# Kernel optimization log

Measured on AMD Instinct MI355X. Metric: run time of the kernel, lower is better.

The kernel has to match this reference:

```python
import jax, jax.numpy as jnp
import numpy as np

SPATIAL_SHAPES = ((100, 100), (50, 50), (25, 25), (13, 13))
B, C, NH, NL, NP, DFF = 4, 256, 8, 4, 4, 1024
HD = C // NH
L = sum(h * w for h, w in SPATIAL_SHAPES)  # 13294


def _xavier(key, shape):
    s = (6.0 / (shape[0] + shape[1])) ** 0.5
    return jax.random.uniform(key, shape, jnp.float32, -s, s)


def setup_inputs():
    key = jax.random.key(0)
    ks = jax.random.split(key, 12)
    ss = jnp.array(SPATIAL_SHAPES, jnp.int32)
    lsi = jnp.concatenate([jnp.zeros((1,), jnp.int32), jnp.cumsum(ss[:, 0] * ss[:, 1])[:-1].astype(jnp.int32)])
    return {
        "query": jax.random.normal(ks[0], (B, L, C), jnp.float32),
        "query_pos": jax.random.normal(ks[1], (B, L, C), jnp.float32),
        "reference_points": jax.random.uniform(ks[2], (B, L, NL, 2), jnp.float32),
        "spatial_shapes": ss,
        "level_start_index": lsi,
        "v_W": _xavier(ks[3], (C, C)), "v_b": jnp.zeros((C,), jnp.float32),
        "off_W": 0.01 * jax.random.normal(ks[4], (C, NH * NL * NP * 2), jnp.float32),
        "off_b": 0.1 * jax.random.normal(ks[5], (NH * NL * NP * 2,), jnp.float32),
        "aw_W": 0.01 * jax.random.normal(ks[6], (C, NH * NL * NP), jnp.float32),
        "aw_b": jnp.zeros((NH * NL * NP,), jnp.float32),
        "out_W": _xavier(ks[7], (C, C)), "out_b": jnp.zeros((C,), jnp.float32),
        "ln1_g": jnp.ones((C,), jnp.float32), "ln1_b": jnp.zeros((C,), jnp.float32),
        "lin1_W": _xavier(ks[8], (C, DFF)), "lin1_b": jnp.zeros((DFF,), jnp.float32),
        "lin2_W": _xavier(ks[9], (DFF, C)), "lin2_b": jnp.zeros((C,), jnp.float32),
        "ln2_g": jnp.ones((C,), jnp.float32), "ln2_b": jnp.zeros((C,), jnp.float32),
    }


def _layer_norm(x, g, b):
    mu = x.mean(-1, keepdims=True)
    var = ((x - mu) ** 2).mean(-1, keepdims=True)
    return (x - mu) * jax.lax.rsqrt(var + 1e-5) * g + b


def _msda(q, value, reference_points, v_W, v_b, off_W, off_b, aw_W, aw_b, out_W, out_b):
    # value projection, split heads -> [B, NH, L, HD]
    v = (value @ v_W + v_b).reshape(B, L, NH, HD).transpose(0, 2, 1, 3)
    off = (q @ off_W + off_b).reshape(B, L, NH, NL, NP, 2)
    aw = jax.nn.softmax((q @ aw_W + aw_b).reshape(B, L, NH, NL * NP), axis=-1)
    aw = aw.reshape(B, L, NH, NL, NP).transpose(0, 2, 1, 3, 4)  # [B,NH,L,NL,NP]
    # offset normalizer is (W, H) per level, matching (x, y) coords
    norm = jnp.array([[w, h] for h, w in SPATIAL_SHAPES], q.dtype)
    loc = reference_points[:, :, None, :, None, :] + off / norm[None, None, None, :, None, :]
    loc = loc.transpose(0, 2, 1, 3, 4, 5)  # [B,NH,L,NL,NP,2]
    acc = jnp.zeros((B, NH, L, HD), q.dtype)
    start = 0
    for l, (H_, W_) in enumerate(SPATIAL_SHAPES):
        v_l = jax.lax.dynamic_slice_in_dim(v, start, H_ * W_, axis=2)  # [B,NH,HW,HD]
        # grid_sample(align_corners=False): pixel = loc*size - 0.5
        x = loc[:, :, :, l, :, 0] * W_ - 0.5  # [B,NH,L,NP]
        y = loc[:, :, :, l, :, 1] * H_ - 0.5
        x0 = jnp.floor(x); y0 = jnp.floor(y)
        lx = x - x0; ly = y - y0
        x0i = x0.astype(jnp.int32); y0i = y0.astype(jnp.int32)

        def corner(yi, xi, w):
            valid = (yi >= 0) & (yi < H_) & (xi >= 0) & (xi < W_)  # zero padding
            idx = jnp.clip(yi, 0, H_ - 1) * W_ + jnp.clip(xi, 0, W_ - 1)
            g = jnp.take_along_axis(v_l, idx.reshape(B, NH, L * NP, 1), axis=2)
            g = g.reshape(B, NH, L, NP, HD)
            return g * (w * valid)[..., None]

        s = (corner(y0i, x0i, (1 - ly) * (1 - lx))
             + corner(y0i, x0i + 1, (1 - ly) * lx)
             + corner(y0i + 1, x0i, ly * (1 - lx))
             + corner(y0i + 1, x0i + 1, ly * lx))  # [B,NH,L,NP,HD]
        acc = acc + (s * aw[:, :, :, l, :, None]).sum(3)
        start += H_ * W_
    out = acc.transpose(0, 2, 1, 3).reshape(B, L, C)
    return out @ out_W + out_b


def _forward(query, query_pos, reference_points, v_W, v_b, off_W, off_b, aw_W, aw_b,
             out_W, out_b, ln1_g, ln1_b, lin1_W, lin1_b, lin2_W, lin2_b, ln2_g, ln2_b):
    q = query + query_pos
    src2 = _msda(q, query, reference_points, v_W, v_b, off_W, off_b, aw_W, aw_b, out_W, out_b)
    x = _layer_norm(query + src2, ln1_g, ln1_b)
    ffn = jax.nn.relu(x @ lin1_W + lin1_b) @ lin2_W + lin2_b
    return _layer_norm(x + ffn, ln2_g, ln2_b)


def reference(query, query_pos, reference_points, spatial_shapes, level_start_index,
              v_W, v_b, off_W, off_b, aw_W, aw_b, out_W, out_b,
              ln1_g, ln1_b, lin1_W, lin1_b, lin2_W, lin2_b, ln2_g, ln2_b):
    # spatial_shapes / level_start_index are consistent with the static SPATIAL_SHAPES
    # constant (shapes must be static for reshapes under jit).
    return _forward(query, query_pos, reference_points, v_W, v_b, off_W, off_b, aw_W, aw_b,
                    out_W, out_b, ln1_g, ln1_b, lin1_W, lin1_b, lin2_W, lin2_b, ln2_g, ln2_b)
```

## Files before the change

kernel.cpp:

```cpp
#include <hip/hip_runtime.h>
#include <hip/hip_bf16.h>
#include <cstddef>

constexpr int Ll   = 13294;
constexpr int NROW = 4 * Ll;
constexpr int MP   = 53248;

typedef __bf16       bf8v __attribute__((ext_vector_type(8)));
typedef __bf16       bf2v __attribute__((ext_vector_type(2)));
typedef float        f4v  __attribute__((ext_vector_type(4)));
typedef unsigned int u4v  __attribute__((ext_vector_type(4)));

#if defined(__has_builtin)
#  if __has_builtin(__builtin_amdgcn_fdot2_f32_bf16)
#    define HAVE_DOT2_BF16 1
#  endif
#endif
#ifndef HAVE_DOT2_BF16
#  define HAVE_DOT2_BF16 0
#endif

__device__ __forceinline__ void xcd_remap(int& m0, int& n0)
{
    const int nwg  = gridDim.x * gridDim.y;
    const int flat = blockIdx.y * gridDim.x + blockIdx.x;
    const int w    = (flat & 7) * (nwg >> 3) + (flat >> 3);
    n0 = (w % gridDim.x) * 128;
    m0 = (w / gridDim.x) * 128;
}

template<bool RELU, bool OUTF, bool OUTB>
__global__ __launch_bounds__(256)
void gemm_mfma(const __hip_bfloat16* __restrict__ A, const __hip_bfloat16* __restrict__ Bt,
               const float* __restrict__ bias, const float* __restrict__ bias2,
               float* __restrict__ Cf, __hip_bfloat16* __restrict__ Cb,
               int M, int N, int K)
{
    __shared__ __hip_bfloat16 As[2][128 * 32];
    __shared__ __hip_bfloat16 Bs[2][128 * 32];
    const int tid  = threadIdx.x;
    const int wid  = tid >> 6;
    const int lane = tid & 63;
    int m0, n0;
    xcd_remap(m0, n0);
    const int wm = wid >> 1, wn = wid & 1;
    const int fr = lane & 15, fq = lane >> 4;
    const int sr = lane >> 2;
    const int sc = (lane & 3) * 8;

    f4v acc[4][4] = {};

    for (int k0 = 0; k0 < K; k0 += 64) {
        #pragma unroll
        for (int h = 0; h < 2; ++h) {
            #pragma unroll
            for (int i = 0; i < 2; ++i) {
                const int s = wid * 2 + i;
                const __hip_bfloat16* sa = A  + (size_t)(m0 + s * 16 + sr) * K + k0 + h * 32 + sc;
                const __hip_bfloat16* sb = Bt + (size_t)(n0 + s * 16 + sr) * K + k0 + h * 32 + sc;
                __builtin_amdgcn_global_load_lds(
                    (const __attribute__((address_space(1))) void*)sa,
                    (__attribute__((address_space(3))) void*)&As[h][s * 512], 16, 0, 0);
                __builtin_amdgcn_global_load_lds(
                    (const __attribute__((address_space(1))) void*)sb,
                    (__attribute__((address_space(3))) void*)&Bs[h][s * 512], 16, 0, 0);
            }
        }
        __syncthreads();

        #pragma unroll
        for (int h = 0; h < 2; ++h) {
            bf8v a[4], b[4];
            #pragma unroll
            for (int r = 0; r < 4; ++r) {
                a[r] = __builtin_bit_cast(bf8v, *(const u4v*)&As[h][(wm * 64 + r * 16 + fr) * 32 + fq * 8]);
                b[r] = __builtin_bit_cast(bf8v, *(const u4v*)&Bs[h][(wn * 64 + r * 16 + fr) * 32 + fq * 8]);
            }
            #pragma unroll
            for (int nr = 0; nr < 4; ++nr)
                #pragma unroll
                for (int mr = 0; mr < 4; ++mr)
                    acc[nr][mr] = __builtin_amdgcn_mfma_f32_16x16x32_bf16(b[nr], a[mr], acc[nr][mr], 0, 0, 0);
        }
        __syncthreads();
    }

    #pragma unroll
    for (int nr = 0; nr < 4; ++nr) {
        const int colbase = n0 + wn * 64 + nr * 16 + fq * 4;
        const float* bp = (bias2 != nullptr && colbase >= 256) ? (bias2 - 256) : bias;
        const float4 b4 = *(const float4*)&bp[colbase];
        #pragma unroll
        for (int mr = 0; mr < 4; ++mr) {
            const int row = m0 + wm * 64 + mr * 16 + fr;
            f4v v = acc[nr][mr];
            v[0] += b4.x; v[1] += b4.y; v[2] += b4.z; v[3] += b4.w;
            if (RELU) {
                v[0] = fmaxf(v[0], 0.f); v[1] = fmaxf(v[1], 0.f);
                v[2] = fmaxf(v[2], 0.f); v[3] = fmaxf(v[3], 0.f);
            }
            if (OUTF)
                *(float4*)&Cf[(size_t)row * N + colbase] = make_float4(v[0], v[1], v[2], v[3]);
            if (OUTB) {
                union { ushort4 u; __hip_bfloat16 h[4]; } pk;
                pk.h[0] = __float2bfloat16(v[0]); pk.h[1] = __float2bfloat16(v[1]);
                pk.h[2] = __float2bfloat16(v[2]); pk.h[3] = __float2bfloat16(v[3]);
                *(ushort4*)&Cb[(size_t)row * N + colbase] = pk.u;
            }
        }
    }
}

template<bool STOREB, bool RESB>
__global__ __launch_bounds__(256)
void gemm_ln(const __hip_bfloat16* __restrict__ A, const __hip_bfloat16* __restrict__ Bt,
             const float* __restrict__ bias,
             const float* __restrict__ resF, const __hip_bfloat16* __restrict__ resB,
             int Mres,
             const float* __restrict__ g, const float* __restrict__ be,
             float* __restrict__ outF, int MstoreF,
             __hip_bfloat16* __restrict__ outB,
             int K)
{
    __shared__ __hip_bfloat16 As[2][64 * 32];
    __shared__ __hip_bfloat16 Bs[2][256 * 32];
    __shared__ float red[2][64][2];
    const int tid  = threadIdx.x;
    const int wid  = tid >> 6;
    const int lane = tid & 63;
    const int m0 = blockIdx.x * 64;
    const int wm = wid >> 1, wn = wid & 1;
    const int fr = lane & 15, fq = lane >> 4;
    const int sr = lane >> 2;
    const int sc = (lane & 3) * 8;

    f4v acc[8][2] = {};

    for (int k0 = 0; k0 < K; k0 += 64) {
        #pragma unroll
        for (int h = 0; h < 2; ++h) {
            {
                const __hip_bfloat16* sa = A + (size_t)(m0 + wid * 16 + sr) * K + k0 + h * 32 + sc;
                __builtin_amdgcn_global_load_lds(
                    (const __attribute__((address_space(1))) void*)sa,
                    (__attribute__((address_space(3))) void*)&As[h][wid * 512], 16, 0, 0);
            }
            #pragma unroll
            for (int i = 0; i < 4; ++i) {
                const int s = wid * 4 + i;
                const __hip_bfloat16* sb = Bt + (size_t)(s * 16 + sr) * K + k0 + h * 32 + sc;
                __builtin_amdgcn_global_load_lds(
                    (const __attribute__((address_space(1))) void*)sb,
                    (__attribute__((address_space(3))) void*)&Bs[h][s * 512], 16, 0, 0);
            }
        }
        __syncthreads();

        #pragma unroll
        for (int h = 0; h < 2; ++h) {
            bf8v a[2], b[8];
            #pragma unroll
            for (int r = 0; r < 2; ++r)
                a[r] = __builtin_bit_cast(bf8v, *(const u4v*)&As[h][(wm * 32 + r * 16 + fr) * 32 + fq * 8]);
            #pragma unroll
            for (int r = 0; r < 8; ++r)
                b[r] = __builtin_bit_cast(bf8v, *(const u4v*)&Bs[h][(wn * 128 + r * 16 + fr) * 32 + fq * 8]);
            #pragma unroll
            for (int nr = 0; nr < 8; ++nr)
                #pragma unroll
                for (int mr = 0; mr < 2; ++mr)
                    acc[nr][mr] = __builtin_amdgcn_mfma_f32_16x16x32_bf16(b[nr], a[mr], acc[nr][mr], 0, 0, 0);
        }
        __syncthreads();
    }

    float s2[2] = {}, q2[2] = {};
    #pragma unroll
    for (int nr = 0; nr < 8; ++nr) {
        const int colbase = wn * 128 + nr * 16 + fq * 4;
        const float4 b4 = *(const float4*)&bias[colbase];
        #pragma unroll
        for (int mr = 0; mr < 2; ++mr) {
            const int row = m0 + wm * 32 + mr * 16 + fr;
            f4v x = acc[nr][mr];
            x[0] += b4.x; x[1] += b4.y; x[2] += b4.z; x[3] += b4.w;
            if (RESB) {
                const ushort4 r4 = *(const ushort4*)&resB[(size_t)row * 256 + colbase];
                x[0] += __builtin_bit_cast(float, (unsigned)r4.x << 16);
                x[1] += __builtin_bit_cast(float, (unsigned)r4.y << 16);
                x[2] += __builtin_bit_cast(float, (unsigned)r4.z << 16);
                x[3] += __builtin_bit_cast(float, (unsigned)r4.w << 16);
            } else if (row < Mres) {
                const float4 r4 = *(const float4*)&resF[(size_t)row * 256 + colbase];
                x[0] += r4.x; x[1] += r4.y; x[2] += r4.z; x[3] += r4.w;
            }
            acc[nr][mr] = x;
            s2[mr] += x[0] + x[1] + x[2] + x[3];
            q2[mr] += x[0]*x[0] + x[1]*x[1] + x[2]*x[2] + x[3]*x[3];
        }
    }
    #pragma unroll
    for (int mr = 0; mr < 2; ++mr) {
        s2[mr] += __shfl_xor(s2[mr], 16, 64);
        q2[mr] += __shfl_xor(q2[mr], 16, 64);
        s2[mr] += __shfl_xor(s2[mr], 32, 64);
        q2[mr] += __shfl_xor(q2[mr], 32, 64);
    }
    if (fq == 0) {
        #pragma unroll
        for (int mr = 0; mr < 2; ++mr) {
            red[wn][wm * 32 + mr * 16 + fr][0] = s2[mr];
            red[wn][wm * 32 + mr * 16 + fr][1] = q2[mr];
        }
    }
    __syncthreads();
    float mean[2], rinv[2];
    #pragma unroll
    for (int mr = 0; mr < 2; ++mr) {
        const int r = wm * 32 + mr * 16 + fr;
        const float ss = red[0][r][0] + red[1][r][0];
        const float qq = red[0][r][1] + red[1][r][1];
        mean[mr] = ss * (1.f / 256.f);
        const float var = qq * (1.f / 256.f) - mean[mr] * mean[mr];
        rinv[mr] = rsqrtf(var + 1e-5f);
    }
    #pragma unroll
    for (int nr = 0; nr < 8; ++nr) {
        const int colbase = wn * 128 + nr * 16 + fq * 4;
        const float4 g4 = *(const float4*)&g[colbase];
        const float4 e4 = *(const float4*)&be[colbase];
        #pragma unroll
        for (int mr = 0; mr < 2; ++mr) {
            const int row = m0 + wm * 32 + mr * 16 + fr;
            const f4v x = acc[nr][mr];
            float y0 = (x[0] - mean[mr]) * rinv[mr] * g4.x + e4.x;
            float y1 = (x[1] - mean[mr]) * rinv[mr] * g4.y + e4.y;
            float y2 = (x[2] - mean[mr]) * rinv[mr] * g4.z + e4.z;
            float y3 = (x[3] - mean[mr]) * rinv[mr] * g4.w + e4.w;
            if (row < MstoreF)
                *(float4*)&outF[(size_t)row * 256 + colbase] = make_float4(y0, y1, y2, y3);
            if (STOREB) {
                union { ushort4 u; __hip_bfloat16 h[4]; } pk;
                pk.h[0] = __float2bfloat16(y0); pk.h[1] = __float2bfloat16(y1);
                pk.h[2] = __float2bfloat16(y2); pk.h[3] = __float2bfloat16(y3);
                *(ushort4*)&outB[(size_t)row * 256 + colbase] = pk.u;
            }
        }
    }
}

__global__ __launch_bounds__(256)
void prep_weights(const float* __restrict__ vW, const float* __restrict__ offW,
                  const float* __restrict__ awW, const float* __restrict__ outW,
                  const float* __restrict__ w1, const float* __restrict__ w2,
                  __hip_bfloat16* __restrict__ vWt, __hip_bfloat16* __restrict__ catWt,
                  __hip_bfloat16* __restrict__ outWt, __hip_bfloat16* __restrict__ w1t,
                  __hip_bfloat16* __restrict__ w2t)
{
    int i = blockIdx.x * 256 + threadIdx.x;
    if (i < 65536) { const int n = i >> 8, k = i & 255;
        vWt[i] = __float2bfloat16(vW[(size_t)k * 256 + n]); return; }
    i -= 65536;
    if (i < 98304) { const int n = i >> 8, k = i & 255;
        catWt[i] = __float2bfloat16(n < 256 ? offW[(size_t)k * 256 + n]
                                            : awW[(size_t)k * 128 + n - 256]); return; }
    i -= 98304;
    if (i < 65536) { const int n = i >> 8, k = i & 255;
        outWt[i] = __float2bfloat16(outW[(size_t)k * 256 + n]); return; }
    i -= 65536;
    if (i < 262144) { const int n = i >> 8, k = i & 255;
        w1t[i] = __float2bfloat16(w1[(size_t)k * 1024 + n]); return; }
    i -= 262144;
    { const int n = i >> 10, k = i & 1023;
        w2t[i] = __float2bfloat16(w2[(size_t)k * 256 + n]); }
}

__global__ __launch_bounds__(256)
void cvt_both(const float* __restrict__ q, const float* __restrict__ qp,
              __hip_bfloat16* __restrict__ qb, __hip_bfloat16* __restrict__ qpb)
{
    const int i   = blockIdx.x * 256 + threadIdx.x;
    const int row = i >> 5;
    union { u4v u; __hip_bfloat16 h[8]; } p1, p2;
    if (row >= NROW) {
        u4v z = {0u, 0u, 0u, 0u};
        p1.u = z; p2.u = z;
    } else {
        const size_t e = (size_t)i * 8;
        float4 x0 = *(const float4*)&q[e];
        float4 x1 = *(const float4*)&q[e + 4];
        float4 y0 = *(const float4*)&qp[e];
        float4 y1 = *(const float4*)&qp[e + 4];
        p1.h[0] = __float2bfloat16(x0.x); p1.h[1] = __float2bfloat16(x0.y);
        p1.h[2] = __float2bfloat16(x0.z); p1.h[3] = __float2bfloat16(x0.w);
        p1.h[4] = __float2bfloat16(x1.x); p1.h[5] = __float2bfloat16(x1.y);
        p1.h[6] = __float2bfloat16(x1.z); p1.h[7] = __float2bfloat16(x1.w);
        p2.h[0] = __float2bfloat16(x0.x + y0.x); p2.h[1] = __float2bfloat16(x0.y + y0.y);
        p2.h[2] = __float2bfloat16(x0.z + y0.z); p2.h[3] = __float2bfloat16(x0.w + y0.w);
        p2.h[4] = __float2bfloat16(x1.x + y1.x); p2.h[5] = __float2bfloat16(x1.y + y1.y);
        p2.h[6] = __float2bfloat16(x1.z + y1.z); p2.h[7] = __float2bfloat16(x1.w + y1.w);
    }
    *(u4v*)&qb[(size_t)i * 8]  = p1.u;
    *(u4v*)&qpb[(size_t)i * 8] = p2.u;
}

__device__ __forceinline__ float blo(unsigned u) { return __builtin_bit_cast(float, u << 16); }
__device__ __forceinline__ float bhi(unsigned u) { return __builtin_bit_cast(float, u & 0xffff0000u); }

__global__ __launch_bounds__(256)
void msda_sample5(const __hip_bfloat16* __restrict__ v, const __hip_bfloat16* __restrict__ cat,
                  const float* __restrict__ refp, __hip_bfloat16* __restrict__ accO)
{
    __shared__ int      sIdx[1024][4];
    __shared__ unsigned sWpk[1024][2];
    int blk;
    {
        const int nwg  = gridDim.x;
        const int q    = nwg >> 3;
        const int r    = nwg & 7;
        const int xcd  = blockIdx.x & 7;
        const int off  = blockIdx.x >> 3;
        blk = (xcd < r ? xcd * (q + 1) : r * (q + 1) + (xcd - r) * q) + off;
    }
    const int row0 = blk * 8;
    const int tid  = threadIdx.x;

    #pragma unroll
    for (int it = 0; it < 4; ++it) {
        const int item = it * 256 + tid;
        const int p = item & 15, h = (item >> 4) & 7, r = item >> 7;
        const int row = row0 + r;
        const int lvl = p >> 2;
        const float logit = __bfloat162float(cat[(size_t)row * 384 + 256 + h * 16 + p]);
        float mx = logit;
        #pragma unroll
        for (int o = 1; o < 16; o <<= 1) mx = fmaxf(mx, __shfl_xor(mx, o, 64));
        const float e = __expf(logit - mx);
        float s = e;
        #pragma unroll
        for (int o = 1; o < 16; o <<= 1) s += __shfl_xor(s, o, 64);
        const float aw = e / s;

        const int Hs_[4] = {100, 50, 25, 13};
        const int Ss[4]  = {0, 10000, 12500, 13125};
        const int   Wl = Hs_[lvl];
        const float Wf = (float)Wl;
        const float ox = __bfloat162float(cat[(size_t)row * 384 + h * 32 + p * 2 + 0]);
        const float oy = __bfloat162float(cat[(size_t)row * 384 + h * 32 + p * 2 + 1]);
        const float rx = refp[(size_t)row * 8 + lvl * 2 + 0];
        const float ry = refp[(size_t)row * 8 + lvl * 2 + 1];
        const float x = (rx + ox / Wf) * Wf - 0.5f;
        const float y = (ry + oy / Wf) * Wf - 0.5f;
        const float x0f = floorf(x), y0f = floorf(y);
        const float lx = x - x0f, ly = y - y0f;
        const int x0 = (int)x0f, y0 = (int)y0f;
        const int b = row / Ll;
        const int vbase = b * Ll + Ss[lvl];
        int ixr[4]; unsigned short wb[4];
        #pragma unroll
        for (int c = 0; c < 4; ++c) {
            const int cy = c >> 1, cx = c & 1;
            const int yi = y0 + cy, xi = x0 + cx;
            const bool ok = (yi >= 0) & (yi < Wl) & (xi >= 0) & (xi < Wl);
            const int yc = min(max(yi, 0), Wl - 1);
            const int xc = min(max(xi, 0), Wl - 1);
            const float wt = (cy ? ly : 1.f - ly) * (cx ? lx : 1.f - lx);
            ixr[c] = (vbase + yc * Wl + xc) * 512;
            const __hip_bfloat16 hw = __float2bfloat16(ok ? aw * wt : 0.f);
            wb[c] = __builtin_bit_cast(unsigned short, hw);
        }
        const int item2 = (item & ~15) | ((item & 15) ^ h);
        *(int4*)&sIdx[item2][0] = make_int4(ixr[0], ixr[1], ixr[2], ixr[3]);
        sWpk[item2][0] = (unsigned)wb[0] | ((unsigned)wb[1] << 16);
        sWpk[item2][1] = (unsigned)wb[2] | ((unsigned)wb[3] << 16);
    }
    __syncthreads();

    const int r   = tid >> 5;
    const int h   = (tid >> 2) & 7;
    const int oct = tid & 3;
    const int row = row0 + r;
    const char* vB = (const char*)v + (h * 32 + oct * 8) * 2;
    const int ibase = r * 128 + h * 16;
    float acc[8] = {};
    #pragma unroll
    for (int i = 0; i < 16; ++i) {
        const int idx = ibase + (i ^ h);
        const int4  ix = *(const int4*)&sIdx[idx][0];
        const uint2 wp = *(const uint2*)&sWpk[idx][0];
        u4v u0 = *(const u4v*)(vB + (unsigned)ix.x);
        u4v u1 = *(const u4v*)(vB + (unsigned)ix.y);
        u4v u2 = *(const u4v*)(vB + (unsigned)ix.z);
        u4v u3 = *(const u4v*)(vB + (unsigned)ix.w);
#if HAVE_DOT2_BF16
        const bf2v w01 = __builtin_bit_cast(bf2v, wp.x);
        const bf2v w23 = __builtin_bit_cast(bf2v, wp.y);
        #pragma unroll
        for (int q = 0; q < 4; ++q) {
            const unsigned lo01 = __builtin_amdgcn_perm(u1[q], u0[q], 0x05040100u);
            const unsigned hi01 = __builtin_amdgcn_perm(u1[q], u0[q], 0x07060302u);
            const unsigned lo23 = __builtin_amdgcn_perm(u3[q], u2[q], 0x05040100u);
            const unsigned hi23 = __builtin_amdgcn_perm(u3[q], u2[q], 0x07060302u);
            acc[2*q]   = __builtin_amdgcn_fdot2_f32_bf16(__builtin_bit_cast(bf2v, lo01), w01, acc[2*q],   false);
            acc[2*q]   = __builtin_amdgcn_fdot2_f32_bf16(__builtin_bit_cast(bf2v, lo23), w23, acc[2*q],   false);
            acc[2*q+1] = __builtin_amdgcn_fdot2_f32_bf16(__builtin_bit_cast(bf2v, hi01), w01, acc[2*q+1], false);
            acc[2*q+1] = __builtin_amdgcn_fdot2_f32_bf16(__builtin_bit_cast(bf2v, hi23), w23, acc[2*q+1], false);
        }
#else
        const float w0 = blo(wp.x), w1 = bhi(wp.x);
        const float w2 = blo(wp.y), w3 = bhi(wp.y);
        #pragma unroll
        for (int q = 0; q < 4; ++q) {
            acc[2*q]   = fmaf(w0, blo(u0[q]), acc[2*q]);
            acc[2*q+1] = fmaf(w0, bhi(u0[q]), acc[2*q+1]);
            acc[2*q]   = fmaf(w1, blo(u1[q]), acc[2*q]);
            acc[2*q+1] = fmaf(w1, bhi(u1[q]), acc[2*q+1]);
            acc[2*q]   = fmaf(w2, blo(u2[q]), acc[2*q]);
            acc[2*q+1] = fmaf(w2, bhi(u2[q]), acc[2*q+1]);
            acc[2*q]   = fmaf(w3, blo(u3[q]), acc[2*q]);
            acc[2*q+1] = fmaf(w3, bhi(u3[q]), acc[2*q+1]);
        }
#endif
    }
    union { u4v u; __hip_bfloat16 hh[8]; } pk;
    #pragma unroll
    for (int q = 0; q < 8; ++q) pk.hh[q] = __float2bfloat16(acc[q]);
    *(u4v*)&accO[(size_t)row * 256 + h * 32 + oct * 8] = pk.u;
}

extern "C" void kernel_launch(void* const* d_in, const int* in_sizes, int n_in,
                              void* d_out, int out_size, void* d_ws, size_t ws_size,
                              hipStream_t stream)
{
    (void)in_sizes; (void)n_in; (void)out_size; (void)ws_size;
    const float* query = (const float*)d_in[0];
    const float* qpos  = (const float*)d_in[1];
    const float* refp  = (const float*)d_in[2];
    const float* v_W   = (const float*)d_in[5];
    const float* v_b   = (const float*)d_in[6];
    const float* off_W = (const float*)d_in[7];
    const float* off_b = (const float*)d_in[8];
    const float* aw_W  = (const float*)d_in[9];
    const float* aw_b  = (const float*)d_in[10];
    const float* out_W = (const float*)d_in[11];
    const float* out_b = (const float*)d_in[12];
    const float* ln1g  = (const float*)d_in[13];
    const float* ln1b  = (const float*)d_in[14];
    const float* w1    = (const float*)d_in[15];
    const float* b1    = (const float*)d_in[16];
    const float* w2    = (const float*)d_in[17];
    const float* b2    = (const float*)d_in[18];
    const float* ln2g  = (const float*)d_in[19];
    const float* ln2b  = (const float*)d_in[20];
    float* out = (float*)d_out;

    char* ws = (char*)d_ws;
    constexpr size_t HALF_B = (size_t)MP * 256 * 2;
    constexpr size_t HBUF_B = (size_t)MP * 1024 * 2;
    __hip_bfloat16* hbuf = (__hip_bfloat16*)ws;
    __hip_bfloat16* qb   = (__hip_bfloat16*)ws;
    __hip_bfloat16* qpb  = (__hip_bfloat16*)(ws + HALF_B);
    __hip_bfloat16* catb = (__hip_bfloat16*)(ws + 2 * HALF_B);
    __hip_bfloat16* vbuf = (__hip_bfloat16*)(ws + HBUF_B);
    __hip_bfloat16* accb = qpb;
    __hip_bfloat16* xb   = vbuf;
    char* wsw = ws + HBUF_B + HALF_B;
    __hip_bfloat16* vWt   = (__hip_bfloat16*)(wsw);
    __hip_bfloat16* catWt = (__hip_bfloat16*)(wsw + 131072);
    __hip_bfloat16* outWt = (__hip_bfloat16*)(wsw + 327680);
    __hip_bfloat16* w1t   = (__hip_bfloat16*)(wsw + 458752);
    __hip_bfloat16* w2t   = (__hip_bfloat16*)(wsw + 983040);

    dim3 blk(256);

    prep_weights<<<2944, blk, 0, stream>>>(v_W, off_W, aw_W, out_W, w1, w2,
                                           vWt, catWt, outWt, w1t, w2t);
    cvt_both<<<MP / 8, blk, 0, stream>>>(query, qpos, qb, qpb);

    gemm_mfma<false, false, true><<<dim3(2, MP / 128), blk, 0, stream>>>(
        qb, vWt, v_b, nullptr, nullptr, vbuf, MP, 256, 256);
    gemm_mfma<false, false, true><<<dim3(3, MP / 128), blk, 0, stream>>>(
        qpb, catWt, off_b, aw_b, nullptr, catb, MP, 384, 256);

    msda_sample5<<<NROW / 8, blk, 0, stream>>>(vbuf, catb, refp, accb);

    gemm_ln<true, true><<<MP / 64, blk, 0, stream>>>(
        accb, outWt, out_b, nullptr, qb, MP, ln1g, ln1b,
        nullptr, 0, xb, 256);

    gemm_mfma<true, false, true><<<dim3(8, MP / 128), blk, 0, stream>>>(
        xb, w1t, b1, nullptr, nullptr, hbuf, MP, 1024, 256);

    gemm_ln<false, true><<<MP / 64, blk, 0, stream>>>(
        hbuf, w2t, b2, nullptr, xb, MP, ln2g, ln2b,
        out, NROW, nullptr, 1024);
}
```

Measured before the change: 343.4 us.

## Merge prep kernels, fuse projection GEMMs, software-pipeline MSDA sampling loads

Three changes ship together. The weight-prep and query-conversion kernels are merged into one launch, and the value and offset/attention projection GEMMs share a single grid with an XCD-aware tile remap, cutting launches and tail idle time. The MSDA sampling loop is now double-buffered: gathers for the next two sampling points are issued before the current ones are consumed, and sched_barriers stop the compiler from reordering them. This raises register pressure and adds branch divergence between the two GEMM shapes in the fused grid.

```diff
diff --git a/kernel.cpp b/kernel.cpp
--- a/kernel.cpp
+++ b/kernel.cpp
@@ -30,19 +30,16 @@
 }
 
 template<bool RELU, bool OUTF, bool OUTB>
-__global__ __launch_bounds__(256)
-void gemm_mfma(const __hip_bfloat16* __restrict__ A, const __hip_bfloat16* __restrict__ Bt,
+__device__ __forceinline__
+void gemm_body(const __hip_bfloat16* __restrict__ A, const __hip_bfloat16* __restrict__ Bt,
                const float* __restrict__ bias, const float* __restrict__ bias2,
                float* __restrict__ Cf, __hip_bfloat16* __restrict__ Cb,
-               int M, int N, int K)
-{
-    __shared__ __hip_bfloat16 As[2][128 * 32];
-    __shared__ __hip_bfloat16 Bs[2][128 * 32];
+               int N, int K, int m0, int n0,
+               __hip_bfloat16 (*As)[128 * 32], __hip_bfloat16 (*Bs)[128 * 32])
+{
     const int tid  = threadIdx.x;
     const int wid  = tid >> 6;
     const int lane = tid & 63;
-    int m0, n0;
-    xcd_remap(m0, n0);
     const int wm = wid >> 1, wn = wid & 1;
     const int fr = lane & 15, fq = lane >> 4;
     const int sr = lane >> 2;
@@ -109,6 +106,41 @@
             }
         }
     }
+}
+
+template<bool RELU, bool OUTF, bool OUTB>
+__global__ __launch_bounds__(256)
+void gemm_mfma(const __hip_bfloat16* __restrict__ A, const __hip_bfloat16* __restrict__ Bt,
+               const float* __restrict__ bias, const float* __restrict__ bias2,
+               float* __restrict__ Cf, __hip_bfloat16* __restrict__ Cb,
+               int M, int N, int K)
+{
+    __shared__ __hip_bfloat16 As[2][128 * 32];
+    __shared__ __hip_bfloat16 Bs[2][128 * 32];
+    int m0, n0;
+    xcd_remap(m0, n0);
+    gemm_body<RELU, OUTF, OUTB>(A, Bt, bias, bias2, Cf, Cb, N, K, m0, n0, As, Bs);
+}
+
+__global__ __launch_bounds__(256)
+void gemm_proj_pair(const __hip_bfloat16* __restrict__ qb, const __hip_bfloat16* __restrict__ qpb,
+                    const __hip_bfloat16* __restrict__ vWt, const __hip_bfloat16* __restrict__ catWt,
+                    const float* __restrict__ v_b, const float* __restrict__ off_b,
+                    const float* __restrict__ aw_b,
+                    __hip_bfloat16* __restrict__ vbuf, __hip_bfloat16* __restrict__ catb)
+{
+    __shared__ __hip_bfloat16 As[2][128 * 32];
+    __shared__ __hip_bfloat16 Bs[2][128 * 32];
+    const int nwg  = 2080;
+    const int flat = blockIdx.x;
+    const int w    = (flat & 7) * (nwg >> 3) + (flat >> 3);
+    const int n    = w % 5, m = w / 5;
+    if (n < 2)
+        gemm_body<false, false, true>(qb, vWt, v_b, nullptr,
+                                      nullptr, vbuf, 256, 256, m * 128, n * 128, As, Bs);
+    else
+        gemm_body<false, false, true>(qpb, catWt, off_b, aw_b,
+                                      nullptr, catb, 384, 256, m * 128, (n - 2) * 128, As, Bs);
 }
 
 template<bool STOREB, bool RESB>
@@ -250,36 +282,35 @@
 }
 
 __global__ __launch_bounds__(256)
-void prep_weights(const float* __restrict__ vW, const float* __restrict__ offW,
-                  const float* __restrict__ awW, const float* __restrict__ outW,
-                  const float* __restrict__ w1, const float* __restrict__ w2,
-                  __hip_bfloat16* __restrict__ vWt, __hip_bfloat16* __restrict__ catWt,
-                  __hip_bfloat16* __restrict__ outWt, __hip_bfloat16* __restrict__ w1t,
-                  __hip_bfloat16* __restrict__ w2t)
-{
-    int i = blockIdx.x * 256 + threadIdx.x;
-    if (i < 65536) { const int n = i >> 8, k = i & 255;
-        vWt[i] = __float2bfloat16(vW[(size_t)k * 256 + n]); return; }
-    i -= 65536;
-    if (i < 98304) { const int n = i >> 8, k = i & 255;
-        catWt[i] = __float2bfloat16(n < 256 ? offW[(size_t)k * 256 + n]
-                                            : awW[(size_t)k * 128 + n - 256]); return; }
-    i -= 98304;
-    if (i < 65536) { const int n = i >> 8, k = i & 255;
-        outWt[i] = __float2bfloat16(outW[(size_t)k * 256 + n]); return; }
-    i -= 65536;
-    if (i < 262144) { const int n = i >> 8, k = i & 255;
-        w1t[i] = __float2bfloat16(w1[(size_t)k * 1024 + n]); return; }
-    i -= 262144;
-    { const int n = i >> 10, k = i & 1023;
-        w2t[i] = __float2bfloat16(w2[(size_t)k * 256 + n]); }
-}
-
-__global__ __launch_bounds__(256)
-void cvt_both(const float* __restrict__ q, const float* __restrict__ qp,
+void prep_all(const float* __restrict__ vW, const float* __restrict__ offW,
+              const float* __restrict__ awW, const float* __restrict__ outW,
+              const float* __restrict__ w1, const float* __restrict__ w2,
+              __hip_bfloat16* __restrict__ vWt, __hip_bfloat16* __restrict__ catWt,
+              __hip_bfloat16* __restrict__ outWt, __hip_bfloat16* __restrict__ w1t,
+              __hip_bfloat16* __restrict__ w2t,
+              const float* __restrict__ q, const float* __restrict__ qp,
               __hip_bfloat16* __restrict__ qb, __hip_bfloat16* __restrict__ qpb)
 {
-    const int i   = blockIdx.x * 256 + threadIdx.x;
+    if (blockIdx.x < 2944) {
+        int i = blockIdx.x * 256 + threadIdx.x;
+        if (i < 65536) { const int n = i >> 8, k = i & 255;
+            vWt[i] = __float2bfloat16(vW[(size_t)k * 256 + n]); return; }
+        i -= 65536;
+        if (i < 98304) { const int n = i >> 8, k = i & 255;
+            catWt[i] = __float2bfloat16(n < 256 ? offW[(size_t)k * 256 + n]
+                                                : awW[(size_t)k * 128 + n - 256]); return; }
+        i -= 98304;
+        if (i < 65536) { const int n = i >> 8, k = i & 255;
+            outWt[i] = __float2bfloat16(outW[(size_t)k * 256 + n]); return; }
+        i -= 65536;
+        if (i < 262144) { const int n = i >> 8, k = i & 255;
+            w1t[i] = __float2bfloat16(w1[(size_t)k * 1024 + n]); return; }
+        i -= 262144;
+        { const int n = i >> 10, k = i & 1023;
+            w2t[i] = __float2bfloat16(w2[(size_t)k * 256 + n]); }
+        return;
+    }
+    const int i   = (blockIdx.x - 2944) * 256 + threadIdx.x;
     const int row = i >> 5;
     union { u4v u; __hip_bfloat16 h[8]; } p1, p2;
     if (row >= NROW) {
@@ -307,8 +338,50 @@
 __device__ __forceinline__ float blo(unsigned u) { return __builtin_bit_cast(float, u << 16); }
 __device__ __forceinline__ float bhi(unsigned u) { return __builtin_bit_cast(float, u & 0xffff0000u); }
 
+#if HAVE_DOT2_BF16
+#define MSDA_CONSUME(WP, U0, U1, U2, U3) do { \
+    const bf2v w01_ = __builtin_bit_cast(bf2v, (WP).x); \
+    const bf2v w23_ = __builtin_bit_cast(bf2v, (WP).y); \
+    _Pragma("unroll") \
+    for (int q_ = 0; q_ < 4; ++q_) { \
+        const unsigned lo01_ = __builtin_amdgcn_perm((U1)[q_], (U0)[q_], 0x05040100u); \
+        const unsigned hi01_ = __builtin_amdgcn_perm((U1)[q_], (U0)[q_], 0x07060302u); \
+        const unsigned lo23_ = __builtin_amdgcn_perm((U3)[q_], (U2)[q_], 0x05040100u); \
+        const unsigned hi23_ = __builtin_amdgcn_perm((U3)[q_], (U2)[q_], 0x07060302u); \
+        acc[2*q_]   = __builtin_amdgcn_fdot2_f32_bf16(__builtin_bit_cast(bf2v, lo01_), w01_, acc[2*q_],   false); \
+        acc[2*q_]   = __builtin_amdgcn_fdot2_f32_bf16(__builtin_bit_cast(bf2v, lo23_), w23_, acc[2*q_],   false); \
+        acc[2*q_+1] = __builtin_amdgcn_fdot2_f32_bf16(__builtin_bit_cast(bf2v, hi01_), w01_, acc[2*q_+1], false); \
+        acc[2*q_+1] = __builtin_amdgcn_fdot2_f32_bf16(__builtin_bit_cast(bf2v, hi23_), w23_, acc[2*q_+1], false); \
+    } } while (0)
+#else
+#define MSDA_CONSUME(WP, U0, U1, U2, U3) do { \
+    const float w0_ = blo((WP).x), w1_ = bhi((WP).x); \
+    const float w2_ = blo((WP).y), w3_ = bhi((WP).y); \
+    _Pragma("unroll") \
+    for (int q_ = 0; q_ < 4; ++q_) { \
+        acc[2*q_]   = fmaf(w0_, blo((U0)[q_]), acc[2*q_]); \
+        acc[2*q_+1] = fmaf(w0_, bhi((U0)[q_]), acc[2*q_+1]); \
+        acc[2*q_]   = fmaf(w1_, blo((U1)[q_]), acc[2*q_]); \
+        acc[2*q_+1] = fmaf(w1_, bhi((U1)[q_]), acc[2*q_+1]); \
+        acc[2*q_]   = fmaf(w2_, blo((U2)[q_]), acc[2*q_]); \
+        acc[2*q_+1] = fmaf(w2_, bhi((U2)[q_]), acc[2*q_+1]); \
+        acc[2*q_]   = fmaf(w3_, blo((U3)[q_]), acc[2*q_]); \
+        acc[2*q_+1] = fmaf(w3_, bhi((U3)[q_]), acc[2*q_+1]); \
+    } } while (0)
+#endif
+
+#define MSDA_LOAD(I, WP, U0, U1, U2, U3) do { \
+    const int idx_ = ibase + ((I) ^ h); \
+    const int4 ix_ = *(const int4*)&sIdx[idx_][0]; \
+    WP = *(const uint2*)&sWpk[idx_][0]; \
+    U0 = *(const u4v*)(vB + (unsigned)ix_.x); \
+    U1 = *(const u4v*)(vB + (unsigned)ix_.y); \
+    U2 = *(const u4v*)(vB + (unsigned)ix_.z); \
+    U3 = *(const u4v*)(vB + (unsigned)ix_.w); \
+} while (0)
+
 __global__ __launch_bounds__(256)
-void msda_sample5(const __hip_bfloat16* __restrict__ v, const __hip_bfloat16* __restrict__ cat,
+void msda_sample6(const __hip_bfloat16* __restrict__ v, const __hip_bfloat16* __restrict__ cat,
                   const float* __restrict__ refp, __hip_bfloat16* __restrict__ accO)
 {
     __shared__ int      sIdx[1024][4];
@@ -383,45 +456,25 @@
     const char* vB = (const char*)v + (h * 32 + oct * 8) * 2;
     const int ibase = r * 128 + h * 16;
     float acc[8] = {};
-    #pragma unroll
-    for (int i = 0; i < 16; ++i) {
-        const int idx = ibase + (i ^ h);
-        const int4  ix = *(const int4*)&sIdx[idx][0];
-        const uint2 wp = *(const uint2*)&sWpk[idx][0];
-        u4v u0 = *(const u4v*)(vB + (unsigned)ix.x);
-        u4v u1 = *(const u4v*)(vB + (unsigned)ix.y);
-        u4v u2 = *(const u4v*)(vB + (unsigned)ix.z);
-        u4v u3 = *(const u4v*)(vB + (unsigned)ix.w);
-#if HAVE_DOT2_BF16
-        const bf2v w01 = __builtin_bit_cast(bf2v, wp.x);
-        const bf2v w23 = __builtin_bit_cast(bf2v, wp.y);
-        #pragma unroll
-        for (int q = 0; q < 4; ++q) {
-            const unsigned lo01 = __builtin_amdgcn_perm(u1[q], u0[q], 0x05040100u);
-            const unsigned hi01 = __builtin_amdgcn_perm(u1[q], u0[q], 0x07060302u);
-            const unsigned lo23 = __builtin_amdgcn_perm(u3[q], u2[q], 0x05040100u);
-            const unsigned hi23 = __builtin_amdgcn_perm(u3[q], u2[q], 0x07060302u);
-            acc[2*q]   = __builtin_amdgcn_fdot2_f32_bf16(__builtin_bit_cast(bf2v, lo01), w01, acc[2*q],   false);
-            acc[2*q]   = __builtin_amdgcn_fdot2_f32_bf16(__builtin_bit_cast(bf2v, lo23), w23, acc[2*q],   false);
-            acc[2*q+1] = __builtin_amdgcn_fdot2_f32_bf16(__builtin_bit_cast(bf2v, hi01), w01, acc[2*q+1], false);
-            acc[2*q+1] = __builtin_amdgcn_fdot2_f32_bf16(__builtin_bit_cast(bf2v, hi23), w23, acc[2*q+1], false);
-        }
-#else
-        const float w0 = blo(wp.x), w1 = bhi(wp.x);
-        const float w2 = blo(wp.y), w3 = bhi(wp.y);
-        #pragma unroll
-        for (int q = 0; q < 4; ++q) {
-            acc[2*q]   = fmaf(w0, blo(u0[q]), acc[2*q]);
-            acc[2*q+1] = fmaf(w0, bhi(u0[q]), acc[2*q+1]);
-            acc[2*q]   = fmaf(w1, blo(u1[q]), acc[2*q]);
-            acc[2*q+1] = fmaf(w1, bhi(u1[q]), acc[2*q+1]);
-            acc[2*q]   = fmaf(w2, blo(u2[q]), acc[2*q]);
-            acc[2*q+1] = fmaf(w2, bhi(u2[q]), acc[2*q+1]);
-            acc[2*q]   = fmaf(w3, blo(u3[q]), acc[2*q]);
-            acc[2*q+1] = fmaf(w3, bhi(u3[q]), acc[2*q+1]);
-        }
-#endif
-    }
+
+    uint2 wpA, wpB;
+    u4v uA0, uA1, uA2, uA3, uB0, uB1, uB2, uB3;
+    MSDA_LOAD(0, wpA, uA0, uA1, uA2, uA3);
+    MSDA_LOAD(1, wpB, uB0, uB1, uB2, uB3);
+    #pragma unroll
+    for (int i = 0; i < 16; i += 2) {
+        MSDA_CONSUME(wpA, uA0, uA1, uA2, uA3);
+        if (i + 2 < 16) {
+            MSDA_LOAD(i + 2, wpA, uA0, uA1, uA2, uA3);
+            __builtin_amdgcn_sched_barrier(0);
+        }
+        MSDA_CONSUME(wpB, uB0, uB1, uB2, uB3);
+        if (i + 3 < 16) {
+            MSDA_LOAD(i + 3, wpB, uB0, uB1, uB2, uB3);
+            __builtin_amdgcn_sched_barrier(0);
+        }
+    }
+
     union { u4v u; __hip_bfloat16 hh[8]; } pk;
     #pragma unroll
     for (int q = 0; q < 8; ++q) pk.hh[q] = __float2bfloat16(acc[q]);
@@ -473,16 +526,14 @@
 
     dim3 blk(256);
 
-    prep_weights<<<2944, blk, 0, stream>>>(v_W, off_W, aw_W, out_W, w1, w2,
-                                           vWt, catWt, outWt, w1t, w2t);
-    cvt_both<<<MP / 8, blk, 0, stream>>>(query, qpos, qb, qpb);
-
-    gemm_mfma<false, false, true><<<dim3(2, MP / 128), blk, 0, stream>>>(
-        qb, vWt, v_b, nullptr, nullptr, vbuf, MP, 256, 256);
-    gemm_mfma<false, false, true><<<dim3(3, MP / 128), blk, 0, stream>>>(
-        qpb, catWt, off_b, aw_b, nullptr, catb, MP, 384, 256);
-
-    msda_sample5<<<NROW / 8, blk, 0, stream>>>(vbuf, catb, refp, accb);
+    prep_all<<<2944 + MP / 8, blk, 0, stream>>>(
+        v_W, off_W, aw_W, out_W, w1, w2, vWt, catWt, outWt, w1t, w2t,
+        query, qpos, qb, qpb);
+
+    gemm_proj_pair<<<2080, blk, 0, stream>>>(
+        qb, qpb, vWt, catWt, v_b, off_b, aw_b, vbuf, catb);
+
+    msda_sample6<<<NROW / 8, blk, 0, stream>>>(vbuf, catb, refp, accb);
 
     gemm_ln<true, true><<<MP / 64, blk, 0, stream>>>(
         accb, outWt, out_b, nullptr, qb, MP, ln1g, ln1b,
```

Result: slower. 402.2 us (+17.1%).
